# Kernel optimization log

Hardware: AMD Instinct MI355X
Metric: run time of the kernel (lower is better)

Reference implementation:

```python
import jax, jax.numpy as jnp
import numpy as np

B, H, W = 64, 512, 512          # batch, image height/width
BH, BW = 8, 8                   # block_size
K = 256                         # n_blocks (codebook size)
L = BH * BW                     # block_len = 64
HT, WT = H // BH, W // BW       # tiles per axis
T = HT * WT                     # tiles_per_img = 4096
BETA = 35.0


def _unfold(img):
    # img: (B, 1, H, W) -> patches (B, T, L), matching torch.nn.Unfold
    # with kernel=stride=(BH,BW): tiles row-major, patch flattened (kh, kw).
    x = img.reshape(B, 1, HT, BH, WT, BW)
    x = x.transpose(0, 2, 4, 1, 3, 5)          # (B, HT, WT, 1, BH, BW)
    return x.reshape(B, T, L)


def _fold(patches):
    # patches: (B, T, L) -> img (B, 1, H, W); exact inverse of _unfold
    # (non-overlapping, so Fold is pure reassembly, no accumulation).
    x = patches.reshape(B, HT, WT, 1, BH, BW)
    x = x.transpose(0, 3, 1, 4, 2, 5)          # (B, 1, HT, BH, WT, BW)
    return x.reshape(B, 1, H, W)


def setup_inputs() -> dict:
    key = jax.random.key(0)
    k1, k2 = jax.random.split(key)
    target_img = jax.random.uniform(k1, (B, 1, H, W), dtype=jnp.float32)
    # Learned codebook parameter (Haar-ish init in the original; values
    # don't change the math being tested).
    blocks = jax.random.uniform(k2, (K, BH, BW), dtype=jnp.float32)
    return {"target_img": target_img, "blocks": blocks}


def reference(target_img, blocks):
    patches = _unfold(target_img).reshape(B * T, L)   # (N, L), N = B*T
    codes = blocks.reshape(K, L)                      # (K, L)

    # Squared distances ||a - b||^2 via the expanded form to avoid
    # materializing the (N, K, L) difference tensor.
    a2 = jnp.sum(patches * patches, axis=-1, keepdims=True)   # (N, 1)
    b2 = jnp.sum(codes * codes, axis=-1)                      # (K,)
    ab = patches @ codes.T                                    # (N, K)
    sqerr = a2 - 2.0 * ab + b2                                # (N, K)

    block_weights = jax.nn.softmax(-BETA * sqerr, axis=-1)    # (N, K)
    uf_reconstructed = block_weights @ codes                  # (N, L)

    reconstructed = _fold(uf_reconstructed.reshape(B, T, L))  # (B,1,H,W)
    choice_penalty = jnp.mean(
        jnp.minimum(block_weights, 1.0 - block_weights)) * K
    return reconstructed, choice_penalty
```

## Files before the change

kernel.cpp:

```cpp
#include <hip/hip_runtime.h>


typedef short short8 __attribute__((ext_vector_type(8)));
typedef float floatx4 __attribute__((ext_vector_type(4)));

namespace {
constexpr float BETA_C = 35.0f;
constexpr float TAU    = 1e-6f;
constexpr float INV_N  = 1.0f / 262144.0f;
constexpr size_t IMG_ELEMS = (size_t)64 * 512 * 512;
constexpr int WB0 = 0;
constexpr int WB1 = 4096;
constexpr int WR  = 0;
constexpr int WS  = 4352;
constexpr int NWORDS = 8192;
}

__device__ __forceinline__ unsigned short f2bf(float x) {
  unsigned u = __float_as_uint(x);
  return (unsigned short)((u + 0x7FFFu + ((u >> 16) & 1u)) >> 16);
}
__device__ __forceinline__ float bf2f(unsigned short h) {
  return __uint_as_float((unsigned)h << 16);
}
__device__ __forceinline__ unsigned pack2(unsigned short lo, unsigned short hi) {
  return (unsigned)lo | ((unsigned)hi << 16);
}
__device__ __forceinline__ void cvt8t(float4 a, float4 b, short8& h, short8& l) {
  float f[8] = {a.x, a.y, a.z, a.w, b.x, b.y, b.z, b.w};
#pragma unroll
  for (int i = 0; i < 8; ++i) {
    unsigned short hh = f2bf(f[i]);
    h[i] = (short)hh;
    float lf = f[i] - bf2f(hh);
    l[i] = (short)(__float_as_uint(lf) >> 16);
  }
}
__device__ __forceinline__ void cp16(const uint4* g, unsigned* l) {
  __builtin_amdgcn_global_load_lds(
      (const __attribute__((address_space(1))) void*)g,
      (__attribute__((address_space(3))) void*)l, 16, 0, 0);
}

__global__ void pack_codes(const float* __restrict__ blk,
                           unsigned* __restrict__ wsBh,
                           unsigned* __restrict__ wsBl,
                           float* __restrict__ wsB2) {
  const int c = threadIdx.x;
  const float* src = blk + c * 64;
  float b2 = 0.f;
#pragma unroll
  for (int g = 0; g < 8; ++g) {
    int slot = c * 8 + (g ^ (c & 7));
#pragma unroll
    for (int t = 0; t < 4; ++t) {
      float v0 = src[g * 8 + 2 * t], v1 = src[g * 8 + 2 * t + 1];
      b2 += v0 * v0 + v1 * v1;
      unsigned short h0 = f2bf(v0), h1 = f2bf(v1);
      unsigned short l0 = f2bf(v0 - bf2f(h0)), l1 = f2bf(v1 - bf2f(h1));
      wsBh[slot * 4 + t] = pack2(h0, h1);
      wsBl[slot * 4 + t] = pack2(l0, l1);
    }
  }
  wsB2[c] = -BETA_C * b2;
}

__global__ __launch_bounds__(256, 5) void recon_kernel(
    const float* __restrict__ img, const float* __restrict__ blk,
    const unsigned* __restrict__ wsBh, const unsigned* __restrict__ wsBl,
    const float* __restrict__ wsB2, float* __restrict__ out,
    float* __restrict__ penAcc) {
  __shared__ unsigned sMem[NWORDS];
  float* sMemF = reinterpret_cast<float*>(sMem);

  const int tid = threadIdx.x;
  const int lane = tid & 63;
  const int wave = tid >> 6;
  const int b = blockIdx.x >> 6;
  const int ht = blockIdx.x & 63;
  const int c15 = lane & 15;
  const int q = lane >> 4;

  const float* imgBase = img + (size_t)b * (512 * 512) + (size_t)(ht * 8) * 512;
  const float* aptr = imgBase + q * 512 + (wave * 16 + c15) * 8;
  float4 v00 = *reinterpret_cast<const float4*>(aptr);
  float4 v01 = *reinterpret_cast<const float4*>(aptr + 4);
  float4 v10 = *reinterpret_cast<const float4*>(aptr + 2048);
  float4 v11 = *reinterpret_cast<const float4*>(aptr + 2048 + 4);

  const uint4* srcH = reinterpret_cast<const uint4*>(wsBh);
  const uint4* srcL = reinterpret_cast<const uint4*>(wsBl);
#pragma unroll
  for (int i = 0; i < 4; ++i) {
    cp16(srcH + i * 256 + tid, &sMem[WB0 + (i * 4 + wave) * 256]);
    cp16(srcL + i * 256 + tid, &sMem[WB1 + (i * 4 + wave) * 256]);
  }

  short8 ah[2], al[2];
  cvt8t(v00, v01, ah[0], al[0]);
  cvt8t(v10, v11, ah[1], al[1]);

  asm volatile("s_waitcnt vmcnt(0)" ::: "memory");
  __syncthreads();

  const int kx = c15 & 7;
  const unsigned* pb0 = &sMem[(8 * c15 + (q ^ kx)) * 4];
  const unsigned* pb1 = &sMem[(8 * c15 + ((q ^ 4) ^ kx)) * 4];

  float m[4], sm[4];
  float rr[16] = {0.f, 0.f, 0.f, 0.f, 0.f, 0.f, 0.f, 0.f,
                  0.f, 0.f, 0.f, 0.f, 0.f, 0.f, 0.f, 0.f};

#pragma unroll
  for (int h = 0; h < 2; ++h) {
    floatx4 acc[8];
#pragma unroll
    for (int n = 0; n < 8; ++n) acc[n] = (floatx4){0.f, 0.f, 0.f, 0.f};
#pragma unroll
    for (int n = 0; n < 8; ++n) {
      short8 b0h = *reinterpret_cast<const short8*>(pb0 + 512 * n);
      short8 b1h = *reinterpret_cast<const short8*>(pb1 + 512 * n);
      short8 b0l = *reinterpret_cast<const short8*>(pb0 + WB1 + 512 * n);
      short8 b1l = *reinterpret_cast<const short8*>(pb1 + WB1 + 512 * n);
      acc[n] = __builtin_amdgcn_mfma_f32_16x16x32_bf16(ah[0], b0h, acc[n], 0, 0, 0);
      acc[n] = __builtin_amdgcn_mfma_f32_16x16x32_bf16(al[0], b0h, acc[n], 0, 0, 0);
      acc[n] = __builtin_amdgcn_mfma_f32_16x16x32_bf16(ah[1], b1h, acc[n], 0, 0, 0);
      acc[n] = __builtin_amdgcn_mfma_f32_16x16x32_bf16(al[1], b1h, acc[n], 0, 0, 0);
      acc[n] = __builtin_amdgcn_mfma_f32_16x16x32_bf16(ah[0], b0l, acc[n], 0, 0, 0);
      acc[n] = __builtin_amdgcn_mfma_f32_16x16x32_bf16(ah[1], b1l, acc[n], 0, 0, 0);
    }
    if (h == 0) {
      __syncthreads();
#pragma unroll
      for (int i = 0; i < 4; ++i) {
        cp16(srcH + 1024 + i * 256 + tid, &sMem[WB0 + (i * 4 + wave) * 256]);
        cp16(srcL + 1024 + i * 256 + tid, &sMem[WB1 + (i * 4 + wave) * 256]);
      }
    }

#pragma unroll
    for (int n = 0; n < 8; ++n) {
      float b2s = wsB2[128 * h + 16 * n + c15];
#pragma unroll
      for (int r = 0; r < 4; ++r)
        acc[n][r] = fmaf(2.0f * BETA_C, acc[n][r], b2s);
    }
    float M[4];
#pragma unroll
    for (int r = 0; r < 4; ++r) {
      float mm = acc[0][r];
#pragma unroll
      for (int n = 1; n < 8; ++n) mm = fmaxf(mm, acc[n][r]);
#pragma unroll
      for (int off = 1; off <= 8; off <<= 1) mm = fmaxf(mm, __shfl_xor(mm, off, 64));
      M[r] = mm;
    }
    if (h == 0) {
#pragma unroll
      for (int r = 0; r < 4; ++r) { m[r] = M[r]; sm[r] = 0.f; }
    } else {
      float scl[4];
#pragma unroll
      for (int r = 0; r < 4; ++r) {
        float mn = fmaxf(m[r], M[r]);
        scl[r] = __expf(m[r] - mn);
        m[r] = mn;
        sm[r] *= scl[r];
      }
#pragma unroll
      for (int qq = 0; qq < 4; ++qq)
#pragma unroll
        for (int r = 0; r < 4; ++r) {
          float sq = __shfl(scl[r], qq * 16 + c15, 64);
          rr[4 * qq + r] *= sq;
        }
    }
#pragma unroll
    for (int n = 0; n < 8; ++n)
#pragma unroll
      for (int r = 0; r < 4; ++r) {
        float e = __expf(acc[n][r] - m[r]);
        acc[n][r] = e;
        sm[r] += e;
      }
#pragma unroll
    for (int n = 0; n < 8; ++n) {
      float em = fmaxf(fmaxf(acc[n][0], acc[n][1]), fmaxf(acc[n][2], acc[n][3]));
      unsigned long long msk = __ballot(em > TAU);
      while (msk) {
        int L = __builtin_ctzll(msk);
        msk &= msk - 1;
        float w0 = __uint_as_float(__builtin_amdgcn_readlane(__float_as_uint(acc[n][0]), L));
        float w1 = __uint_as_float(__builtin_amdgcn_readlane(__float_as_uint(acc[n][1]), L));
        float w2 = __uint_as_float(__builtin_amdgcn_readlane(__float_as_uint(acc[n][2]), L));
        float w3 = __uint_as_float(__builtin_amdgcn_readlane(__float_as_uint(acc[n][3]), L));
        float bv = blk[(size_t)(128 * h + 16 * n + (L & 15)) * 64 + lane];
        switch (L >> 4) {
          case 0: rr[0] += w0 * bv;  rr[1] += w1 * bv;  rr[2] += w2 * bv;  rr[3] += w3 * bv;  break;
          case 1: rr[4] += w0 * bv;  rr[5] += w1 * bv;  rr[6] += w2 * bv;  rr[7] += w3 * bv;  break;
          case 2: rr[8] += w0 * bv;  rr[9] += w1 * bv;  rr[10] += w2 * bv; rr[11] += w3 * bv; break;
          default: rr[12] += w0 * bv; rr[13] += w1 * bv; rr[14] += w2 * bv; rr[15] += w3 * bv; break;
        }
      }
    }
    if (h == 0) {
      asm volatile("s_waitcnt vmcnt(0)" ::: "memory");
      __syncthreads();
    }
  }

  float invS[4];
#pragma unroll
  for (int r = 0; r < 4; ++r) {
#pragma unroll
    for (int off = 1; off <= 8; off <<= 1) sm[r] += __shfl_xor(sm[r], off, 64);
    invS[r] = 1.0f / sm[r];
  }
  float pen = 0.f;
  if (c15 == 0) {
#pragma unroll
    for (int r = 0; r < 4; ++r)
      pen += (invS[r] > 0.5f) ? (2.0f - 2.0f * invS[r]) : 1.0f;
  }
  pen += __shfl_xor(pen, 16, 64);
  pen += __shfl_xor(pen, 32, 64);
  if (lane == 0) atomicAdd(penAcc, pen * INV_N);

  __syncthreads();

  if (c15 == 0) {
#pragma unroll
    for (int r = 0; r < 4; ++r)
      sMemF[WS + wave * 16 + 4 * q + r] = invS[r];
  }
#pragma unroll
  for (int pl = 0; pl < 16; ++pl)
    sMemF[WR + (wave * 16 + pl) * 68 + lane] = rr[pl];
  float* outBase = out + (size_t)b * (512 * 512) + (size_t)(ht * 8) * 512 +
                   wave * 128;
#pragma unroll
  for (int i = 0; i < 4; ++i) {
    int f = i * 64 + lane;
    int row = f >> 5;
    int cc = f & 31;
    int wtl = cc >> 1, hw = cc & 1;
    float4 v = *reinterpret_cast<const float4*>(
        &sMemF[WR + (wave * 16 + wtl) * 68 + row * 8 + hw * 4]);
    float is = sMemF[WS + wave * 16 + wtl];
    v.x *= is; v.y *= is; v.z *= is; v.w *= is;
    *reinterpret_cast<float4*>(outBase + row * 512 + cc * 4) = v;
  }
}

extern "C" void kernel_launch(void* const* d_in, const int* in_sizes, int n_in,
                              void* d_out, int out_size, void* d_ws, size_t ws_size,
                              hipStream_t stream) {
  const float* img = (const float*)d_in[0];
  const float* blk = (const float*)d_in[1];
  float* out = (float*)d_out;
  float* penSlot = out + IMG_ELEMS;

  unsigned* wsBh = (unsigned*)d_ws;
  unsigned* wsBl = wsBh + 8192;
  float* wsB2 = (float*)(wsBl + 8192);

  pack_codes<<<dim3(1), dim3(256), 0, stream>>>(blk, wsBh, wsBl, wsB2);
  hipMemsetAsync(penSlot, 0, sizeof(float), stream);
  recon_kernel<<<dim3(4096), dim3(256), 0, stream>>>(img, blk, wsBh, wsBl,
                                                     wsB2, out, penSlot);
}
```

Measured before the change: 347.2 us.

## Split codebook staging into four quarter-chunks with double-buffered LDS prefetch

The codebook is now staged in four 64-code quarters across two LDS buffers instead of two 128-code halves in one buffer. Partial vmcnt waits let compute on the current quarter overlap the load of the next one. It also skips rescaling the rr accumulators when no running max changed. The cost is more barriers and more online-softmax merge steps, and vmcnt(4) relies on an exact count of outstanding loads.

Result: slower. 376.6 us (+8.5%).

```diff
diff --git a/kernel.cpp b/kernel.cpp
--- a/kernel.cpp
+++ b/kernel.cpp
@@ -9,8 +9,8 @@
 constexpr float TAU    = 1e-6f;
 constexpr float INV_N  = 1.0f / 262144.0f;
 constexpr size_t IMG_ELEMS = (size_t)64 * 512 * 512;
-constexpr int WB0 = 0;
-constexpr int WB1 = 4096;
+constexpr int WQ0 = 0;
+constexpr int WQ1 = 4096;
 constexpr int WR  = 0;
 constexpr int WS  = 4352;
 constexpr int NWORDS = 8192;
@@ -81,6 +81,9 @@
   const int c15 = lane & 15;
   const int q = lane >> 4;
 
+  const uint4* srcH = reinterpret_cast<const uint4*>(wsBh);
+  const uint4* srcL = reinterpret_cast<const uint4*>(wsBl);
+
   const float* imgBase = img + (size_t)b * (512 * 512) + (size_t)(ht * 8) * 512;
   const float* aptr = imgBase + q * 512 + (wave * 16 + c15) * 8;
   float4 v00 = *reinterpret_cast<const float4*>(aptr);
@@ -88,40 +91,45 @@
   float4 v10 = *reinterpret_cast<const float4*>(aptr + 2048);
   float4 v11 = *reinterpret_cast<const float4*>(aptr + 2048 + 4);
 
-  const uint4* srcH = reinterpret_cast<const uint4*>(wsBh);
-  const uint4* srcL = reinterpret_cast<const uint4*>(wsBl);
-#pragma unroll
-  for (int i = 0; i < 4; ++i) {
-    cp16(srcH + i * 256 + tid, &sMem[WB0 + (i * 4 + wave) * 256]);
-    cp16(srcL + i * 256 + tid, &sMem[WB1 + (i * 4 + wave) * 256]);
+#pragma unroll
+  for (int i = 0; i < 2; ++i) {
+    cp16(srcH + i * 256 + tid, &sMem[WQ0 + (i * 4 + wave) * 256]);
+    cp16(srcL + i * 256 + tid, &sMem[WQ0 + 2048 + (i * 4 + wave) * 256]);
+  }
+#pragma unroll
+  for (int i = 0; i < 2; ++i) {
+    cp16(srcH + 512 + i * 256 + tid, &sMem[WQ1 + (i * 4 + wave) * 256]);
+    cp16(srcL + 512 + i * 256 + tid, &sMem[WQ1 + 2048 + (i * 4 + wave) * 256]);
   }
 
   short8 ah[2], al[2];
   cvt8t(v00, v01, ah[0], al[0]);
   cvt8t(v10, v11, ah[1], al[1]);
 
-  asm volatile("s_waitcnt vmcnt(0)" ::: "memory");
-  __syncthreads();
-
   const int kx = c15 & 7;
-  const unsigned* pb0 = &sMem[(8 * c15 + (q ^ kx)) * 4];
-  const unsigned* pb1 = &sMem[(8 * c15 + ((q ^ 4) ^ kx)) * 4];
+  const int off0 = (8 * c15 + (q ^ kx)) * 4;
+  const int off1 = (8 * c15 + ((q ^ 4) ^ kx)) * 4;
 
   float m[4], sm[4];
   float rr[16] = {0.f, 0.f, 0.f, 0.f, 0.f, 0.f, 0.f, 0.f,
                   0.f, 0.f, 0.f, 0.f, 0.f, 0.f, 0.f, 0.f};
 
 #pragma unroll
-  for (int h = 0; h < 2; ++h) {
-    floatx4 acc[8];
-#pragma unroll
-    for (int n = 0; n < 8; ++n) acc[n] = (floatx4){0.f, 0.f, 0.f, 0.f};
-#pragma unroll
-    for (int n = 0; n < 8; ++n) {
-      short8 b0h = *reinterpret_cast<const short8*>(pb0 + 512 * n);
-      short8 b1h = *reinterpret_cast<const short8*>(pb1 + 512 * n);
-      short8 b0l = *reinterpret_cast<const short8*>(pb0 + WB1 + 512 * n);
-      short8 b1l = *reinterpret_cast<const short8*>(pb1 + WB1 + 512 * n);
+  for (int k = 0; k < 4; ++k) {
+    const int W = (k & 1) ? WQ1 : WQ0;
+    if (k < 3) asm volatile("s_waitcnt vmcnt(4)" ::: "memory");
+    else       asm volatile("s_waitcnt vmcnt(0)" ::: "memory");
+    __syncthreads();
+
+    floatx4 acc[4];
+#pragma unroll
+    for (int n = 0; n < 4; ++n) acc[n] = (floatx4){0.f, 0.f, 0.f, 0.f};
+#pragma unroll
+    for (int n = 0; n < 4; ++n) {
+      short8 b0h = *reinterpret_cast<const short8*>(&sMem[W + off0 + 512 * n]);
+      short8 b1h = *reinterpret_cast<const short8*>(&sMem[W + off1 + 512 * n]);
+      short8 b0l = *reinterpret_cast<const short8*>(&sMem[W + 2048 + off0 + 512 * n]);
+      short8 b1l = *reinterpret_cast<const short8*>(&sMem[W + 2048 + off1 + 512 * n]);
       acc[n] = __builtin_amdgcn_mfma_f32_16x16x32_bf16(ah[0], b0h, acc[n], 0, 0, 0);
       acc[n] = __builtin_amdgcn_mfma_f32_16x16x32_bf16(al[0], b0h, acc[n], 0, 0, 0);
       acc[n] = __builtin_amdgcn_mfma_f32_16x16x32_bf16(ah[1], b1h, acc[n], 0, 0, 0);
@@ -129,18 +137,18 @@
       acc[n] = __builtin_amdgcn_mfma_f32_16x16x32_bf16(ah[0], b0l, acc[n], 0, 0, 0);
       acc[n] = __builtin_amdgcn_mfma_f32_16x16x32_bf16(ah[1], b1l, acc[n], 0, 0, 0);
     }
-    if (h == 0) {
+    if (k < 2) {
       __syncthreads();
 #pragma unroll
-      for (int i = 0; i < 4; ++i) {
-        cp16(srcH + 1024 + i * 256 + tid, &sMem[WB0 + (i * 4 + wave) * 256]);
-        cp16(srcL + 1024 + i * 256 + tid, &sMem[WB1 + (i * 4 + wave) * 256]);
-      }
-    }
-
-#pragma unroll
-    for (int n = 0; n < 8; ++n) {
-      float b2s = wsB2[128 * h + 16 * n + c15];
+      for (int i = 0; i < 2; ++i) {
+        cp16(srcH + (k + 2) * 512 + i * 256 + tid, &sMem[W + (i * 4 + wave) * 256]);
+        cp16(srcL + (k + 2) * 512 + i * 256 + tid, &sMem[W + 2048 + (i * 4 + wave) * 256]);
+      }
+    }
+
+#pragma unroll
+    for (int n = 0; n < 4; ++n) {
+      float b2s = wsB2[64 * k + 16 * n + c15];
 #pragma unroll
       for (int r = 0; r < 4; ++r)
         acc[n][r] = fmaf(2.0f * BETA_C, acc[n][r], b2s);
@@ -148,14 +156,12 @@
     float M[4];
 #pragma unroll
     for (int r = 0; r < 4; ++r) {
-      float mm = acc[0][r];
-#pragma unroll
-      for (int n = 1; n < 8; ++n) mm = fmaxf(mm, acc[n][r]);
+      float mm = fmaxf(fmaxf(acc[0][r], acc[1][r]), fmaxf(acc[2][r], acc[3][r]));
 #pragma unroll
       for (int off = 1; off <= 8; off <<= 1) mm = fmaxf(mm, __shfl_xor(mm, off, 64));
       M[r] = mm;
     }
-    if (h == 0) {
+    if (k == 0) {
 #pragma unroll
       for (int r = 0; r < 4; ++r) { m[r] = M[r]; sm[r] = 0.f; }
     } else {
@@ -167,16 +173,19 @@
         m[r] = mn;
         sm[r] *= scl[r];
       }
-#pragma unroll
-      for (int qq = 0; qq < 4; ++qq)
-#pragma unroll
-        for (int r = 0; r < 4; ++r) {
-          float sq = __shfl(scl[r], qq * 16 + c15, 64);
-          rr[4 * qq + r] *= sq;
-        }
-    }
-#pragma unroll
-    for (int n = 0; n < 8; ++n)
+      bool moved = (scl[0] < 1.f) | (scl[1] < 1.f) | (scl[2] < 1.f) | (scl[3] < 1.f);
+      if (__any(moved)) {
+#pragma unroll
+        for (int qq = 0; qq < 4; ++qq)
+#pragma unroll
+          for (int r = 0; r < 4; ++r) {
+            float sq = __shfl(scl[r], qq * 16 + c15, 64);
+            rr[4 * qq + r] *= sq;
+          }
+      }
+    }
+#pragma unroll
+    for (int n = 0; n < 4; ++n)
 #pragma unroll
       for (int r = 0; r < 4; ++r) {
         float e = __expf(acc[n][r] - m[r]);
@@ -184,7 +193,7 @@
         sm[r] += e;
       }
 #pragma unroll
-    for (int n = 0; n < 8; ++n) {
+    for (int n = 0; n < 4; ++n) {
       float em = fmaxf(fmaxf(acc[n][0], acc[n][1]), fmaxf(acc[n][2], acc[n][3]));
       unsigned long long msk = __ballot(em > TAU);
       while (msk) {
@@ -194,7 +203,7 @@
         float w1 = __uint_as_float(__builtin_amdgcn_readlane(__float_as_uint(acc[n][1]), L));
         float w2 = __uint_as_float(__builtin_amdgcn_readlane(__float_as_uint(acc[n][2]), L));
         float w3 = __uint_as_float(__builtin_amdgcn_readlane(__float_as_uint(acc[n][3]), L));
-        float bv = blk[(size_t)(128 * h + 16 * n + (L & 15)) * 64 + lane];
+        float bv = blk[(size_t)(64 * k + 16 * n + (L & 15)) * 64 + lane];
         switch (L >> 4) {
           case 0: rr[0] += w0 * bv;  rr[1] += w1 * bv;  rr[2] += w2 * bv;  rr[3] += w3 * bv;  break;
           case 1: rr[4] += w0 * bv;  rr[5] += w1 * bv;  rr[6] += w2 * bv;  rr[7] += w3 * bv;  break;
@@ -202,10 +211,6 @@
           default: rr[12] += w0 * bv; rr[13] += w1 * bv; rr[14] += w2 * bv; rr[15] += w3 * bv; break;
         }
       }
-    }
-    if (h == 0) {
-      asm volatile("s_waitcnt vmcnt(0)" ::: "memory");
-      __syncthreads();
     }
   }
 
```
